# Kernel tuning notes

Measured on AMD Instinct MI355X. Metric: run time of the kernel, lower is better.

The kernel has to match this reference:

```python
import jax, jax.numpy as jnp
import numpy as np

B, H, S, D = 4, 16, 2048, 64


def setup_inputs() -> dict:
    key = jax.random.key(0)
    kq, kk, kv = jax.random.split(key, 3)
    q = jax.random.normal(kq, (B, H, S, D), dtype=jnp.float32)
    k = jax.random.normal(kk, (B, H, S, D), dtype=jnp.float32)
    v = jax.random.normal(kv, (B, H, S, D), dtype=jnp.float32)
    return {"q": q, "k": k, "v": v, "num_k": 170}


def reference(q, k, v, num_k):
    d_tensor = k.shape[-1]
    # [B,H,S,S] score matrix
    score = jnp.einsum("bhqd,bhkd->bhqk", q, k) / jnp.sqrt(jnp.float32(d_tensor))
    nk = min(int(num_k), k.shape[2])
    if nk:
        # kth-largest value per query row acts as threshold
        top_vals = jax.lax.top_k(score, nk)[0]          # [B,H,S,nk]
        thresh = top_vals[..., -1:]                      # [B,H,S,1]
        score = jnp.where(score < thresh, jnp.float32(-1e18), score)
    attn = jax.nn.softmax(score, axis=-1)
    return jnp.einsum("bhqk,bhkd->bhqd", attn, v)
```

## Files before the change

### kernel.cpp

```cpp
#include <hip/hip_runtime.h>
#include <math.h>

#define S_LEN 2048
#define DHEAD 64
#define NBINS 512
#define BPL (NBINS / 64)
#define CANDMAX 48
#define NBH 64
#define NROWS (NBH * S_LEN)
#define VT_BYTES (64ull * DHEAD * S_LEN * 2)

typedef _Float16 f16x8 __attribute__((ext_vector_type(8)));
typedef _Float16 f16x4 __attribute__((ext_vector_type(4)));
typedef float    f32x4 __attribute__((ext_vector_type(4)));

__global__ __launch_bounds__(256)
void prep_vt(const float* __restrict__ V, _Float16* __restrict__ VT) {
  __shared__ _Float16 trans[64][72];
  const int bh  = (int)blockIdx.x >> 5;
  const int kt  = (int)blockIdx.x & 31;
  const int t   = (int)threadIdx.x;
  const int key0 = kt * 64;
  const float* Vb = V + ((size_t)bh * S_LEN + key0) * DHEAD;

  {
    const int key = t >> 2;
    const int dc  = t & 3;
    #pragma unroll
    for (int i = 0; i < 4; ++i) {
      int d = dc * 16 + i * 4;
      float4 v4 = *(const float4*)(Vb + (size_t)key * DHEAD + d);
      trans[d + 0][key] = (_Float16)v4.x;
      trans[d + 1][key] = (_Float16)v4.y;
      trans[d + 2][key] = (_Float16)v4.z;
      trans[d + 3][key] = (_Float16)v4.w;
    }
  }
  __syncthreads();

  {
    const int dim = t >> 2;
    const int kc  = t & 3;
    _Float16* dst = VT + ((size_t)bh * DHEAD + dim) * S_LEN + key0 + kc * 16;
    f16x8 a, b;
    #pragma unroll
    for (int j = 0; j < 8; ++j) { a[j] = trans[dim][kc * 16 + j];
                                  b[j] = trans[dim][kc * 16 + 8 + j]; }
    *(f16x8*)(dst)     = a;
    *(f16x8*)(dst + 8) = b;
  }
}

__global__ __launch_bounds__(256, 4)
void qk_kernel(const float* __restrict__ Q, const float* __restrict__ K,
               float* __restrict__ Sws, int row0) {
  __shared__ __align__(16) char kbuf[32768];
  f16x8* Khw = (f16x8*)kbuf;
  f16x8* Klw = (f16x8*)(kbuf + 16384);

  const int tid  = (int)threadIdx.x;
  const int lane = tid & 63;
  const int wid  = tid >> 6;
  const int nxl  = (int)gridDim.x >> 3;
  const int xcd  = (int)blockIdx.x & 7;
  const int lb   = (int)blockIdx.x >> 3;
  const int rb   = lb >> 3;
  const int kb   = lb & 7;
  const int rowl = xcd * (nxl * 8) + rb * 64 + wid * 16;
  const int rowg = row0 + rowl;
  const int bh   = rowg >> 11;
  const int key0 = kb * 256;

  const int g = lane >> 4;
  const int m = lane & 15;

  f16x8 a_hi0, a_lo0, a_hi1, a_lo1;
  {
    const float* Qrow = Q + (size_t)(rowg + m) * DHEAD;
    float4 qa = *(const float4*)(Qrow + g * 8);
    float4 qb = *(const float4*)(Qrow + g * 8 + 4);
    float4 qc = *(const float4*)(Qrow + 32 + g * 8);
    float4 qd = *(const float4*)(Qrow + 32 + g * 8 + 4);
    float x[16] = {qa.x,qa.y,qa.z,qa.w, qb.x,qb.y,qb.z,qb.w,
                   qc.x,qc.y,qc.z,qc.w, qd.x,qd.y,qd.z,qd.w};
    #pragma unroll
    for (int j = 0; j < 8; ++j) {
      _Float16 h0 = (_Float16)x[j];
      a_hi0[j] = h0;  a_lo0[j] = (_Float16)(x[j] - (float)h0);
      _Float16 h1 = (_Float16)x[8 + j];
      a_hi1[j] = h1;  a_lo1[j] = (_Float16)(x[8 + j] - (float)h1);
    }
  }

  const float* Kb = K + (size_t)bh * (S_LEN * DHEAD);
  float* Srow = Sws + (size_t)rowl * S_LEN;

  const int skey  = tid >> 1;
  const int shalf = tid & 1;
  const int ssw   = skey & 7;

  float4 pf[8];
  {
    const float4* kr = (const float4*)(Kb + (size_t)(key0 + skey) * DHEAD + shalf * 32);
    #pragma unroll
    for (int j = 0; j < 8; ++j) pf[j] = kr[j];
  }

  #pragma unroll
  for (int t = 0; t < 2; ++t) {
    #pragma unroll
    for (int jj = 0; jj < 4; ++jj) {
      float x[8] = {pf[2*jj].x, pf[2*jj].y, pf[2*jj].z, pf[2*jj].w,
                    pf[2*jj+1].x, pf[2*jj+1].y, pf[2*jj+1].z, pf[2*jj+1].w};
      f16x8 hi, lo;
      #pragma unroll
      for (int j = 0; j < 8; ++j) {
        _Float16 h = (_Float16)x[j];
        hi[j] = h;
        lo[j] = (_Float16)(x[j] - (float)h);
      }
      int c = shalf * 4 + jj;
      Khw[skey * 8 + (c ^ ssw)] = hi;
      Klw[skey * 8 + (c ^ ssw)] = lo;
    }
    if (t + 1 < 2) {
      const float4* kr = (const float4*)(Kb + (size_t)(key0 + 128 + skey) * DHEAD + shalf * 32);
      #pragma unroll
      for (int j = 0; j < 8; ++j) pf[j] = kr[j];
    }
    __syncthreads();

    const f16x8* Kh = (const f16x8*)kbuf;
    const f16x8* Kl = (const f16x8*)(kbuf + 16384);
    int slot0 = ( g      ^ (m & 7));
    int slot1 = ((4 + g) ^ (m & 7));
    #pragma unroll
    for (int p = 0; p < 8; ++p) {
      int keyr = p * 16 + m;
      f16x8 b_hi0 = Kh[keyr * 8 + slot0];
      f16x8 b_hi1 = Kh[keyr * 8 + slot1];
      f16x8 b_lo0 = Kl[keyr * 8 + slot0];
      f16x8 b_lo1 = Kl[keyr * 8 + slot1];
      f32x4 acc = {0.f, 0.f, 0.f, 0.f};
      acc = __builtin_amdgcn_mfma_f32_16x16x32_f16(a_hi0, b_hi0, acc, 0, 0, 0);
      acc = __builtin_amdgcn_mfma_f32_16x16x32_f16(a_hi1, b_hi1, acc, 0, 0, 0);
      acc = __builtin_amdgcn_mfma_f32_16x16x32_f16(a_hi0, b_lo0, acc, 0, 0, 0);
      acc = __builtin_amdgcn_mfma_f32_16x16x32_f16(a_hi1, b_lo1, acc, 0, 0, 0);
      acc = __builtin_amdgcn_mfma_f32_16x16x32_f16(a_lo0, b_hi0, acc, 0, 0, 0);
      acc = __builtin_amdgcn_mfma_f32_16x16x32_f16(a_lo1, b_hi1, acc, 0, 0, 0);
      acc = __builtin_amdgcn_mfma_f32_16x16x32_f16(a_lo0, b_lo0, acc, 0, 0, 0);
      acc = __builtin_amdgcn_mfma_f32_16x16x32_f16(a_lo1, b_lo1, acc, 0, 0, 0);
      int col = key0 + t * 128 + p * 16 + m;
      #pragma unroll
      for (int rg = 0; rg < 4; ++rg)
        __builtin_nontemporal_store(acc[rg] * 0.125f,
            &Srow[(size_t)(g * 4 + rg) * S_LEN + col]);
    }
    __syncthreads();
  }
}

__global__ __launch_bounds__(512, 4)
void selmm_kernel(const float* __restrict__ Sws, const _Float16* __restrict__ VT,
                  const int* __restrict__ nkp, float* __restrict__ Out, int row0) {
  __shared__ unsigned histS[8][NBINS];
  __shared__ float candS[8][CANDMAX];
  __shared__ unsigned candCnt[8];
  __shared__ float psumS[16];
  __shared__ __align__(16) char pbuf[8192];
  __shared__ __align__(16) float4 redS[4][64];

  const int tid  = (int)threadIdx.x;
  const int lane = tid & 63;
  const int wid  = tid >> 6;
  const int nxl  = (int)gridDim.x >> 3;
  const int xcd  = (int)blockIdx.x & 7;
  const int lbk  = (int)blockIdx.x >> 3;
  const int rowlb = xcd * (nxl * 16) + lbk * 16;
  const int rowgb = row0 + rowlb;
  const int bh    = rowgb >> 11;

  int nk = nkp[0];
  if (nk > S_LEN) nk = S_LEN;

  unsigned* hw = histS[wid];
  float sarr[2][32];
  float thr2[2], vmx2[2];

  #pragma unroll
  for (int rr = 0; rr < 2; ++rr) {
    const int rloc = wid * 2 + rr;
    {
      const f32x4* S4 = (const f32x4*)(Sws + (size_t)(rowlb + rloc) * S_LEN);
      #pragma unroll
      for (int j = 0; j < 8; ++j) {
        f32x4 v4 = __builtin_nontemporal_load(S4 + j * 64 + lane);
        sarr[rr][j*4+0] = v4[0]; sarr[rr][j*4+1] = v4[1];
        sarr[rr][j*4+2] = v4[2]; sarr[rr][j*4+3] = v4[3];
      }
    }

    float vmax = -INFINITY, vmin = INFINITY;
    #pragma unroll
    for (int q = 0; q < 32; ++q) {
      vmax = fmaxf(vmax, sarr[rr][q]); vmin = fminf(vmin, sarr[rr][q]);
    }
    #pragma unroll
    for (int off = 32; off >= 1; off >>= 1) {
      vmax = fmaxf(vmax, __shfl_xor(vmax, off));
      vmin = fminf(vmin, __shfl_xor(vmin, off));
    }

    float thresh = -INFINITY;
    if (nk > 0) {
      float range = vmax - vmin;
      float scale = (range > 0.f) ? ((float)NBINS / range) : 0.f;
      float boff  = vmin * scale;

      #pragma unroll
      for (int i2 = 0; i2 < BPL; ++i2) hw[(i2 << 6) | lane] = 0u;
      #pragma unroll
      for (int q = 0; q < 32; ++q) {
        int bb = (int)fmaf(sarr[rr][q], scale, -boff);
        bb = bb < 0 ? 0 : (bb > NBINS - 1 ? NBINS - 1 : bb);
        atomicAdd(&hw[((bb & 7) << 6) | (bb >> 3)], 1u);
      }

      unsigned A = 0;
      #pragma unroll
      for (int i2 = 0; i2 < BPL; ++i2) A += hw[(i2 << 6) | lane];
      unsigned ssum = A;
      #pragma unroll
      for (int off = 1; off <= 32; off <<= 1) {
        unsigned u = (unsigned)__shfl_down((int)ssum, off);
        if (lane + off < 64) ssum += u;
      }
      unsigned cum = ssum - A;
      int bsel = -1; int mloc = 0; int nbloc = 0;
      #pragma unroll
      for (int i2 = BPL - 1; i2 >= 0; --i2) {
        unsigned c0 = cum; cum += hw[(i2 << 6) | lane];
        if (bsel < 0 && c0 < (unsigned)nk && cum >= (unsigned)nk) {
          bsel = (lane << 3) | i2; mloc = nk - (int)c0; nbloc = (int)(cum - c0);
        }
      }
      unsigned long long fm = __ballot(bsel >= 0);
      int srcl = __ffsll(fm) - 1;
      bsel = __shfl(bsel, srcl);
      int mth  = __shfl(mloc, srcl);
      int nbin = __shfl(nbloc, srcl);

      if (nbin <= CANDMAX) {
        if (lane == 0) candCnt[wid] = 0u;
        __builtin_amdgcn_wave_barrier();
        #pragma unroll
        for (int q = 0; q < 32; ++q) {
          int bb = (int)fmaf(sarr[rr][q], scale, -boff);
          bb = bb < 0 ? 0 : (bb > NBINS - 1 ? NBINS - 1 : bb);
          if (bb == bsel) {
            unsigned ix = atomicAdd(&candCnt[wid], 1u);
            if (ix < CANDMAX) candS[wid][ix] = sarr[rr][q];
          }
        }
        __builtin_amdgcn_wave_barrier();
        float prev = INFINITY, kth = -INFINITY;
        int got = 0, guard = 0;
        while (got < mth && guard++ <= CANDMAX) {
          float best = -INFINITY;
          for (int i = 0; i < nbin; ++i) {
            float v = candS[wid][i];
            if (v < prev && v > best) best = v;
          }
          int ce = 0;
          for (int i = 0; i < nbin; ++i) if (candS[wid][i] == best) ce++;
          got += ce; prev = best; kth = best;
        }
        thresh = kth;
      } else {
        unsigned inbin = 0;
        #pragma unroll
        for (int q = 0; q < 32; ++q) {
          int bb = (int)fmaf(sarr[rr][q], scale, -boff);
          bb = bb < 0 ? 0 : (bb > NBINS - 1 ? NBINS - 1 : bb);
          if (bb == bsel) inbin |= (1u << q);
        }
        while (true) {
          float cmax = -INFINITY;
          #pragma unroll
          for (int q = 0; q < 32; ++q) if (inbin & (1u << q)) cmax = fmaxf(cmax, sarr[rr][q]);
          #pragma unroll
          for (int off = 32; off >= 1; off >>= 1) cmax = fmaxf(cmax, __shfl_xor(cmax, off));
          int cnt = 0;
          #pragma unroll
          for (int q = 0; q < 32; ++q) if ((inbin & (1u << q)) && sarr[rr][q] == cmax) cnt++;
          #pragma unroll
          for (int off = 32; off >= 1; off >>= 1) cnt += __shfl_xor(cnt, off);
          if (mth <= cnt) { thresh = cmax; break; }
          mth -= cnt;
          #pragma unroll
          for (int q = 0; q < 32; ++q) if ((inbin & (1u << q)) && sarr[rr][q] == cmax) inbin &= ~(1u << q);
        }
      }
    }
    thr2[rr] = thresh; vmx2[rr] = vmax;

    float psum = 0.f;
    #pragma unroll
    for (int q = 0; q < 32; ++q) {
      float s = sarr[rr][q];
      psum += (s >= thresh) ? __expf(s - vmax) : 0.f;
    }
    #pragma unroll
    for (int off = 32; off >= 1; off >>= 1) psum += __shfl_xor(psum, off);
    if (lane == 0) psumS[rloc] = psum;
  }
  __syncthreads();

  const int g   = lane >> 4;
  const int n16 = lane & 15;
  const int dg  = wid & 3;
  const int kh  = wid >> 2;
  const _Float16* VTb = VT + (size_t)bh * (DHEAD * S_LEN);
  f32x4 acc = {0.f, 0.f, 0.f, 0.f};

  #pragma unroll
  for (int kt = 0; kt < 8; ++kt) {
    #pragma unroll
    for (int rr = 0; rr < 2; ++rr) {
      const int row = wid * 2 + rr;
      f16x4 pv;
      #pragma unroll
      for (int c = 0; c < 4; ++c) {
        float s = sarr[rr][kt * 4 + c];
        float p = (s >= thr2[rr]) ? __expf(s - vmx2[rr]) : 0.f;
        pv[c] = (_Float16)p;
      }
      *(f16x4*)(pbuf + ((row * 512 + lane * 8) ^ ((row & 7) << 4))) = pv;
    }
    __syncthreads();
    #pragma unroll
    for (int s = 0; s < 4; ++s) {
      f16x8 af = *(const f16x8*)(pbuf +
          ((n16 * 512 + kh * 256 + s * 64 + g * 16) ^ ((n16 & 7) << 4)));
      f16x8 bf = *(const f16x8*)(VTb + (size_t)(dg * 16 + n16) * S_LEN +
                                 kt * 256 + kh * 128 + s * 32 + g * 8);
      acc = __builtin_amdgcn_mfma_f32_16x16x32_f16(af, bf, acc, 0, 0, 0);
    }
    __syncthreads();
  }

  if (kh == 1) {
    redS[dg][lane] = make_float4(acc[0], acc[1], acc[2], acc[3]);
  }
  __syncthreads();
  if (kh == 0) {
    float4 o = redS[dg][lane];
    float ov[4] = {o.x, o.y, o.z, o.w};
    #pragma unroll
    for (int rg = 0; rg < 4; ++rg) {
      int row = g * 4 + rg;
      float val = (acc[rg] + ov[rg]) / psumS[row];
      Out[(size_t)(rowgb + row) * DHEAD + dg * 16 + n16] = val;
    }
  }
}

#define TQ 16
#define KT 128
#define NTILES (S_LEN / KT)
#define THREADS 512
#define LCAP 256
#define SOFF   0
#define KHI    131072
#define KLO    147456
#define HOFF   131072
#define KLOFF  147456
#define PLOFF  155648

__global__ __launch_bounds__(THREADS, 2)
void dpsa_kernel(const float* __restrict__ Q, const float* __restrict__ K,
                 const float* __restrict__ V, const int* __restrict__ nkp,
                 float* __restrict__ Out) {
  __shared__ __align__(16) char smem[163840];
  float* Sf = (float*)(smem + SOFF);

  const int tid  = (int)threadIdx.x;
  const int lane = tid & 63;
  const int wid  = tid >> 6;
  const int bid  = (int)blockIdx.x;
  const int bh   = bid >> 7;
  const int qblk = bid & 127;
  const size_t base = (size_t)bh * (size_t)(S_LEN * DHEAD);
  const float* Kbh = K + base;
  const float* Vbh = V + base;

  int nk = nkp[0];
  if (nk > S_LEN) nk = S_LEN;

  const int g = lane >> 4;
  const int m = lane & 15;

  f16x8 a_hi0, a_lo0, a_hi1, a_lo1;
  {
    const float* Qrow = Q + base + (size_t)(qblk * TQ + m) * DHEAD;
    float4 qa = *(const float4*)(Qrow + g * 8);
    float4 qb = *(const float4*)(Qrow + g * 8 + 4);
    float4 qc = *(const float4*)(Qrow + 32 + g * 8);
    float4 qd = *(const float4*)(Qrow + 32 + g * 8 + 4);
    float x[16] = {qa.x,qa.y,qa.z,qa.w, qb.x,qb.y,qb.z,qb.w,
                   qc.x,qc.y,qc.z,qc.w, qd.x,qd.y,qd.z,qd.w};
    #pragma unroll
    for (int j = 0; j < 8; ++j) {
      _Float16 h0 = (_Float16)x[j];
      a_hi0[j] = h0;  a_lo0[j] = (_Float16)(x[j] - (float)h0);
      _Float16 h1 = (_Float16)x[8 + j];
      a_hi1[j] = h1;  a_lo1[j] = (_Float16)(x[8 + j] - (float)h1);
    }
  }

  const f16x8* Kh = (const f16x8*)(smem + KHI);
  const f16x8* Kl = (const f16x8*)(smem + KLO);
  const int keyl = tid >> 2;
  const int q4i  = tid & 3;
  const int sw   = keyl & 7;

  float4 pf0, pf1, pf2, pf3;
  {
    const float4* Kg4 = (const float4*)Kbh;
    int idx = keyl * 16 + q4i * 4;
    pf0 = Kg4[idx]; pf1 = Kg4[idx + 1]; pf2 = Kg4[idx + 2]; pf3 = Kg4[idx + 3];
  }

  for (int t = 0; t < NTILES; ++t) {
    {
      float x[16] = {pf0.x,pf0.y,pf0.z,pf0.w, pf1.x,pf1.y,pf1.z,pf1.w,
                     pf2.x,pf2.y,pf2.z,pf2.w, pf3.x,pf3.y,pf3.z,pf3.w};
      f16x8 hi0, hi1, lo0, lo1;
      #pragma unroll
      for (int j = 0; j < 8; ++j) {
        _Float16 h0 = (_Float16)x[j];
        hi0[j] = h0;  lo0[j] = (_Float16)(x[j] - (float)h0);
        _Float16 h1 = (_Float16)x[8 + j];
        hi1[j] = h1;  lo1[j] = (_Float16)(x[8 + j] - (float)h1);
      }
      f16x8* KhwF = (f16x8*)(smem + KHI);
      f16x8* KlwF = (f16x8*)(smem + KLO);
      KhwF[keyl * 8 + ((q4i * 2)     ^ sw)] = hi0;
      KhwF[keyl * 8 + ((q4i * 2 + 1) ^ sw)] = hi1;
      KlwF[keyl * 8 + ((q4i * 2)     ^ sw)] = lo0;
      KlwF[keyl * 8 + ((q4i * 2 + 1) ^ sw)] = lo1;
    }
    if (t + 1 < NTILES) {
      const float4* Kg4 = (const float4*)(Kbh + (size_t)(t + 1) * (KT * DHEAD));
      int idx = keyl * 16 + q4i * 4;
      pf0 = Kg4[idx]; pf1 = Kg4[idx + 1]; pf2 = Kg4[idx + 2]; pf3 = Kg4[idx + 3];
    }
    __syncthreads();
    {
      int keyr = wid * 16 + m;
      int s0 = ( g      ^ (m & 7));
      int s1 = ((4 + g) ^ (m & 7));
      f16x8 b_hi0 = Kh[keyr * 8 + s0];
      f16x8 b_hi1 = Kh[keyr * 8 + s1];
      f16x8 b_lo0 = Kl[keyr * 8 + s0];
      f16x8 b_lo1 = Kl[keyr * 8 + s1];
      f32x4 acc = {0.f, 0.f, 0.f, 0.f};
      acc = __builtin_amdgcn_mfma_f32_16x16x32_f16(a_hi0, b_hi0, acc, 0, 0, 0);
      acc = __builtin_amdgcn_mfma_f32_16x16x32_f16(a_hi1, b_hi1, acc, 0, 0, 0);
      acc = __builtin_amdgcn_mfma_f32_16x16x32_f16(a_hi0, b_lo0, acc, 0, 0, 0);
      acc = __builtin_amdgcn_mfma_f32_16x16x32_f16(a_hi1, b_lo1, acc, 0, 0, 0);
      acc = __builtin_amdgcn_mfma_f32_16x16x32_f16(a_lo0, b_hi0, acc, 0, 0, 0);
      acc = __builtin_amdgcn_mfma_f32_16x16x32_f16(a_lo1, b_hi1, acc, 0, 0, 0);
      int keyabs = t * KT + wid * 16 + m;
      #pragma unroll
      for (int rg = 0; rg < 4; ++rg)
        Sf[(size_t)(g * 4 + rg) * S_LEN + keyabs] = acc[rg] * 0.125f;
    }
    __syncthreads();
  }

  unsigned* hw = (unsigned*)(smem + HOFF)  + wid * NBINS;
  unsigned* kl = (unsigned*)(smem + KLOFF) + wid * LCAP;
  float*    pl = (float*)(smem + PLOFF)    + wid * LCAP;
  const float4* S4 = (const float4*)(smem + SOFF);

  for (int rr = 0; rr < 2; ++rr) {
    const int row = wid * 2 + rr;
    float sarr[32];
    #pragma unroll
    for (int j = 0; j < 8; ++j) {
      float4 v4 = S4[row * (S_LEN / 4) + j * 64 + lane];
      sarr[j*4+0] = v4.x; sarr[j*4+1] = v4.y;
      sarr[j*4+2] = v4.z; sarr[j*4+3] = v4.w;
    }

    float vmax = -INFINITY, vmin = INFINITY;
    #pragma unroll
    for (int q = 0; q < 32; ++q) {
      vmax = fmaxf(vmax, sarr[q]); vmin = fminf(vmin, sarr[q]);
    }
    #pragma unroll
    for (int off = 32; off >= 1; off >>= 1) {
      vmax = fmaxf(vmax, __shfl_xor(vmax, off));
      vmin = fminf(vmin, __shfl_xor(vmin, off));
    }

    float thresh = -INFINITY;
    if (nk > 0) {
      float range = vmax - vmin;
      float scale = (range > 0.f) ? ((float)NBINS / range) : 0.f;
      #pragma unroll
      for (int i2 = 0; i2 < BPL; ++i2) hw[(i2 << 6) | lane] = 0u;
      #pragma unroll
      for (int q = 0; q < 32; ++q) {
        int bb = (int)((sarr[q] - vmin) * scale);
        bb = bb < 0 ? 0 : (bb > NBINS - 1 ? NBINS - 1 : bb);
        atomicAdd(&hw[((bb & 7) << 6) | (bb >> 3)], 1u);
      }
      unsigned A = 0; unsigned hv[BPL];
      #pragma unroll
      for (int i2 = 0; i2 < BPL; ++i2) { hv[i2] = hw[(i2 << 6) | lane]; A += hv[i2]; }
      unsigned ssum = A;
      #pragma unroll
      for (int off = 1; off <= 32; off <<= 1) {
        unsigned u = (unsigned)__shfl_down((int)ssum, off);
        if (lane + off < 64) ssum += u;
      }
      unsigned cum = ssum - A;
      int bsel = -1; int mloc = 0;
      #pragma unroll
      for (int i2 = BPL - 1; i2 >= 0; --i2) {
        unsigned c0 = cum; cum += hv[i2];
        if (bsel < 0 && c0 < (unsigned)nk && cum >= (unsigned)nk) {
          bsel = (lane << 3) | i2; mloc = nk - (int)c0;
        }
      }
      unsigned long long fmk = __ballot(bsel >= 0);
      int srcl = __ffsll(fmk) - 1;
      bsel = __shfl(bsel, srcl);
      int mth = __shfl(mloc, srcl);

      unsigned inbin = 0;
      #pragma unroll
      for (int q = 0; q < 32; ++q) {
        int bb = (int)((sarr[q] - vmin) * scale);
        bb = bb < 0 ? 0 : (bb > NBINS - 1 ? NBINS - 1 : bb);
        if (bb == bsel) inbin |= (1u << q);
      }
      while (true) {
        float cmax = -INFINITY;
        #pragma unroll
        for (int q = 0; q < 32; ++q) if (inbin & (1u << q)) cmax = fmaxf(cmax, sarr[q]);
        #pragma unroll
        for (int off = 32; off >= 1; off >>= 1) cmax = fmaxf(cmax, __shfl_xor(cmax, off));
        int cnt = 0;
        #pragma unroll
        for (int q = 0; q < 32; ++q) if ((inbin & (1u << q)) && sarr[q] == cmax) cnt++;
        #pragma unroll
        for (int off = 32; off >= 1; off >>= 1) cnt += __shfl_xor(cnt, off);
        if (mth <= cnt) { thresh = cmax; break; }
        mth -= cnt;
        #pragma unroll
        for (int q = 0; q < 32; ++q) if ((inbin & (1u << q)) && sarr[q] == cmax) inbin &= ~(1u << q);
      }
    }

    float psum = 0.f;
    #pragma unroll
    for (int q = 0; q < 32; ++q) {
      float p = (sarr[q] >= thresh) ? expf(sarr[q] - vmax) : 0.f;
      sarr[q] = p; psum += p;
    }
    #pragma unroll
    for (int off = 32; off >= 1; off >>= 1) psum += __shfl_xor(psum, off);

    unsigned nkept = 0;
    #pragma unroll
    for (int q = 0; q < 32; ++q) {
      bool keep = sarr[q] > 0.f;
      unsigned long long mk = __ballot(keep);
      if (keep) {
        unsigned idx = nkept + (unsigned)__popcll(mk & ((1ull << lane) - 1ull));
        if (idx < LCAP) {
          kl[idx] = (unsigned)((q >> 2) * 256 + lane * 4 + (q & 3));
          pl[idx] = sarr[q];
        }
      }
      nkept += (unsigned)__popcll(mk);
    }

    float acc0 = 0.f, acc1 = 0.f, acc2 = 0.f, acc3 = 0.f;
    if (nkept <= LCAP) {
      unsigned i = 0;
      for (; i + 4 <= nkept; i += 4) {
        acc0 = fmaf(pl[i+0], Vbh[(size_t)kl[i+0] * DHEAD + lane], acc0);
        acc1 = fmaf(pl[i+1], Vbh[(size_t)kl[i+1] * DHEAD + lane], acc1);
        acc2 = fmaf(pl[i+2], Vbh[(size_t)kl[i+2] * DHEAD + lane], acc2);
        acc3 = fmaf(pl[i+3], Vbh[(size_t)kl[i+3] * DHEAD + lane], acc3);
      }
      for (; i < nkept; ++i)
        acc0 = fmaf(pl[i], Vbh[(size_t)kl[i] * DHEAD + lane], acc0);
    } else {
      #pragma unroll
      for (int q = 0; q < 32; ++q) {
        for (int sl = 0; sl < 64; ++sl) {
          float pp = __shfl(sarr[q], sl);
          if (pp > 0.f)
            acc0 = fmaf(pp, Vbh[(size_t)((q >> 2) * 256 + sl * 4 + (q & 3)) * DHEAD + lane], acc0);
        }
      }
    }
    float accv = (acc0 + acc1) + (acc2 + acc3);
    Out[base + (size_t)(qblk * TQ + row) * DHEAD + lane] = accv / psum;
  }
}

extern "C" void kernel_launch(void* const* d_in, const int* in_sizes, int n_in,
                              void* d_out, int out_size, void* d_ws, size_t ws_size,
                              hipStream_t stream) {
  const float* q  = (const float*)d_in[0];
  const float* k  = (const float*)d_in[1];
  const float* v  = (const float*)d_in[2];
  const int*   nk = (const int*)d_in[3];
  float* out = (float*)d_out;

  size_t srem = (ws_size > VT_BYTES) ? (ws_size - VT_BYTES) : 0;
  size_t maxrows = srem / ((size_t)S_LEN * sizeof(float));
  long long chunk = (long long)(maxrows / 512) * 512;
  if (chunk > NROWS) chunk = NROWS;

  if (chunk >= 512) {
    _Float16* vt = (_Float16*)d_ws;
    float* sws = (float*)((char*)d_ws + VT_BYTES);
    prep_vt<<<dim3(2048), dim3(256), 0, stream>>>(v, vt);
    for (int row0 = 0; row0 < NROWS; row0 += (int)chunk) {
      int rows = (NROWS - row0 < (int)chunk) ? (NROWS - row0) : (int)chunk;
      qk_kernel<<<dim3(rows / 8), dim3(256), 0, stream>>>(q, k, sws, row0);
      selmm_kernel<<<dim3(rows / 16), dim3(512), 0, stream>>>(sws, vt, nk, out, row0);
    }
  } else {
    dpsa_kernel<<<dim3(8192), dim3(THREADS), 0, stream>>>(q, k, v, nk, out);
  }
}
```

Baseline: 874.2 us.

## Use one wave per row in selmm with 1024-thread blocks and 4-way K split

The selection and PV kernel now runs 16 waves per block, one score row per wave, where before 8 waves each handled two rows serially. The PV matmul is split four ways over the key dimension and the partial sums are reduced through shared memory. Shared buffers are aliased into one union to fit 16 per-wave histograms. This roughly halves the per-wave register array and serial threshold work, trading it for more threads per block, a lower blocks-per-CU bound, and a larger cross-wave reduction.

After: 1.044 ms. 19.4% more time.

```diff
diff --git a/kernel.cpp b/kernel.cpp
--- a/kernel.cpp
+++ b/kernel.cpp
@@ -37,7 +37,6 @@
     }
   }
   __syncthreads();
-
   {
     const int dim = t >> 2;
     const int kc  = t & 3;
@@ -160,15 +159,16 @@
   }
 }
 
-__global__ __launch_bounds__(512, 4)
+__global__ __launch_bounds__(1024, 2)
 void selmm_kernel(const float* __restrict__ Sws, const _Float16* __restrict__ VT,
                   const int* __restrict__ nkp, float* __restrict__ Out, int row0) {
-  __shared__ unsigned histS[8][NBINS];
-  __shared__ float candS[8][CANDMAX];
-  __shared__ unsigned candCnt[8];
-  __shared__ float psumS[16];
-  __shared__ __align__(16) char pbuf[8192];
-  __shared__ __align__(16) float4 redS[4][64];
+  __shared__ __align__(16) char smem[35968];
+  unsigned* histS  = (unsigned*)smem;
+  char*     pbuf   = smem;
+  float4*   redS   = (float4*)(smem + 8192);
+  float*    candS  = (float*)(smem + 32768);
+  unsigned* candCnt= (unsigned*)(smem + 35840);
+  float*    psumS  = (float*)(smem + 35904);
 
   const int tid  = (int)threadIdx.x;
   const int lane = tid & 63;
@@ -183,183 +183,185 @@
   int nk = nkp[0];
   if (nk > S_LEN) nk = S_LEN;
 
-  unsigned* hw = histS[wid];
-  float sarr[2][32];
-  float thr2[2], vmx2[2];
-
+  unsigned* hw = histS + wid * NBINS;
+  float*    cw = candS + wid * CANDMAX;
+  float sarr[32];
+  float thr, vmx;
+
+  {
+    const f32x4* S4 = (const f32x4*)(Sws + (size_t)(rowlb + wid) * S_LEN);
+    #pragma unroll
+    for (int j = 0; j < 8; ++j) {
+      f32x4 v4 = __builtin_nontemporal_load(S4 + j * 64 + lane);
+      sarr[j*4+0] = v4[0]; sarr[j*4+1] = v4[1];
+      sarr[j*4+2] = v4[2]; sarr[j*4+3] = v4[3];
+    }
+  }
+
+  float vmax = -INFINITY, vmin = INFINITY;
   #pragma unroll
-  for (int rr = 0; rr < 2; ++rr) {
-    const int rloc = wid * 2 + rr;
-    {
-      const f32x4* S4 = (const f32x4*)(Sws + (size_t)(rowlb + rloc) * S_LEN);
-      #pragma unroll
-      for (int j = 0; j < 8; ++j) {
-        f32x4 v4 = __builtin_nontemporal_load(S4 + j * 64 + lane);
-        sarr[rr][j*4+0] = v4[0]; sarr[rr][j*4+1] = v4[1];
-        sarr[rr][j*4+2] = v4[2]; sarr[rr][j*4+3] = v4[3];
-      }
-    }
-
-    float vmax = -INFINITY, vmin = INFINITY;
+  for (int q = 0; q < 32; ++q) {
+    vmax = fmaxf(vmax, sarr[q]); vmin = fminf(vmin, sarr[q]);
+  }
+  #pragma unroll
+  for (int off = 32; off >= 1; off >>= 1) {
+    vmax = fmaxf(vmax, __shfl_xor(vmax, off));
+    vmin = fminf(vmin, __shfl_xor(vmin, off));
+  }
+
+  float thresh = -INFINITY;
+  if (nk > 0) {
+    float range = vmax - vmin;
+    float scale = (range > 0.f) ? ((float)NBINS / range) : 0.f;
+    float boff  = vmin * scale;
+
+    #pragma unroll
+    for (int i2 = 0; i2 < BPL; ++i2) hw[(i2 << 6) | lane] = 0u;
     #pragma unroll
     for (int q = 0; q < 32; ++q) {
-      vmax = fmaxf(vmax, sarr[rr][q]); vmin = fminf(vmin, sarr[rr][q]);
-    }
-    #pragma unroll
-    for (int off = 32; off >= 1; off >>= 1) {
-      vmax = fmaxf(vmax, __shfl_xor(vmax, off));
-      vmin = fminf(vmin, __shfl_xor(vmin, off));
-    }
-
-    float thresh = -INFINITY;
-    if (nk > 0) {
-      float range = vmax - vmin;
-      float scale = (range > 0.f) ? ((float)NBINS / range) : 0.f;
-      float boff  = vmin * scale;
-
-      #pragma unroll
-      for (int i2 = 0; i2 < BPL; ++i2) hw[(i2 << 6) | lane] = 0u;
+      int bb = (int)fmaf(sarr[q], scale, -boff);
+      bb = bb < 0 ? 0 : (bb > NBINS - 1 ? NBINS - 1 : bb);
+      atomicAdd(&hw[((bb & 7) << 6) | (bb >> 3)], 1u);
+    }
+
+    unsigned A = 0;
+    #pragma unroll
+    for (int i2 = 0; i2 < BPL; ++i2) A += hw[(i2 << 6) | lane];
+    unsigned ssum = A;
+    #pragma unroll
+    for (int off = 1; off <= 32; off <<= 1) {
+      unsigned u = (unsigned)__shfl_down((int)ssum, off);
+      if (lane + off < 64) ssum += u;
+    }
+    unsigned cum = ssum - A;
+    int bsel = -1; int mloc = 0; int nbloc = 0;
+    #pragma unroll
+    for (int i2 = BPL - 1; i2 >= 0; --i2) {
+      unsigned c0 = cum; cum += hw[(i2 << 6) | lane];
+      if (bsel < 0 && c0 < (unsigned)nk && cum >= (unsigned)nk) {
+        bsel = (lane << 3) | i2; mloc = nk - (int)c0; nbloc = (int)(cum - c0);
+      }
+    }
+    unsigned long long fm = __ballot(bsel >= 0);
+    int srcl = __ffsll(fm) - 1;
+    bsel = __shfl(bsel, srcl);
+    int mth  = __shfl(mloc, srcl);
+    int nbin = __shfl(nbloc, srcl);
+
+    if (nbin <= CANDMAX) {
+      if (lane == 0) candCnt[wid] = 0u;
+      __builtin_amdgcn_wave_barrier();
       #pragma unroll
       for (int q = 0; q < 32; ++q) {
-        int bb = (int)fmaf(sarr[rr][q], scale, -boff);
+        int bb = (int)fmaf(sarr[q], scale, -boff);
         bb = bb < 0 ? 0 : (bb > NBINS - 1 ? NBINS - 1 : bb);
-        atomicAdd(&hw[((bb & 7) << 6) | (bb >> 3)], 1u);
-      }
-
-      unsigned A = 0;
-      #pragma unroll
-      for (int i2 = 0; i2 < BPL; ++i2) A += hw[(i2 << 6) | lane];
-      unsigned ssum = A;
-      #pragma unroll
-      for (int off = 1; off <= 32; off <<= 1) {
-        unsigned u = (unsigned)__shfl_down((int)ssum, off);
-        if (lane + off < 64) ssum += u;
-      }
-      unsigned cum = ssum - A;
-      int bsel = -1; int mloc = 0; int nbloc = 0;
-      #pragma unroll
-      for (int i2 = BPL - 1; i2 >= 0; --i2) {
-        unsigned c0 = cum; cum += hw[(i2 << 6) | lane];
-        if (bsel < 0 && c0 < (unsigned)nk && cum >= (unsigned)nk) {
-          bsel = (lane << 3) | i2; mloc = nk - (int)c0; nbloc = (int)(cum - c0);
+        if (bb == bsel) {
+          unsigned ix = atomicAdd(&candCnt[wid], 1u);
+          if (ix < CANDMAX) cw[ix] = sarr[q];
         }
       }
-      unsigned long long fm = __ballot(bsel >= 0);
-      int srcl = __ffsll(fm) - 1;
-      bsel = __shfl(bsel, srcl);
-      int mth  = __shfl(mloc, srcl);
-      int nbin = __shfl(nbloc, srcl);
-
-      if (nbin <= CANDMAX) {
-        if (lane == 0) candCnt[wid] = 0u;
-        __builtin_amdgcn_wave_barrier();
-        #pragma unroll
-        for (int q = 0; q < 32; ++q) {
-          int bb = (int)fmaf(sarr[rr][q], scale, -boff);
-          bb = bb < 0 ? 0 : (bb > NBINS - 1 ? NBINS - 1 : bb);
-          if (bb == bsel) {
-            unsigned ix = atomicAdd(&candCnt[wid], 1u);
-            if (ix < CANDMAX) candS[wid][ix] = sarr[rr][q];
-          }
+      __builtin_amdgcn_wave_barrier();
+      float prev = INFINITY, kth = -INFINITY;
+      int got = 0, guard = 0;
+      while (got < mth && guard++ <= CANDMAX) {
+        float best = -INFINITY;
+        for (int i = 0; i < nbin; ++i) {
+          float v = cw[i];
+          if (v < prev && v > best) best = v;
         }
-        __builtin_amdgcn_wave_barrier();
-        float prev = INFINITY, kth = -INFINITY;
-        int got = 0, guard = 0;
-        while (got < mth && guard++ <= CANDMAX) {
-          float best = -INFINITY;
-          for (int i = 0; i < nbin; ++i) {
-            float v = candS[wid][i];
-            if (v < prev && v > best) best = v;
-          }
-          int ce = 0;
-          for (int i = 0; i < nbin; ++i) if (candS[wid][i] == best) ce++;
-          got += ce; prev = best; kth = best;
-        }
-        thresh = kth;
-      } else {
-        unsigned inbin = 0;
-        #pragma unroll
-        for (int q = 0; q < 32; ++q) {
-          int bb = (int)fmaf(sarr[rr][q], scale, -boff);
-          bb = bb < 0 ? 0 : (bb > NBINS - 1 ? NBINS - 1 : bb);
-          if (bb == bsel) inbin |= (1u << q);
-        }
-        while (true) {
-          float cmax = -INFINITY;
-          #pragma unroll
-          for (int q = 0; q < 32; ++q) if (inbin & (1u << q)) cmax = fmaxf(cmax, sarr[rr][q]);
-          #pragma unroll
-          for (int off = 32; off >= 1; off >>= 1) cmax = fmaxf(cmax, __shfl_xor(cmax, off));
-          int cnt = 0;
-          #pragma unroll
-          for (int q = 0; q < 32; ++q) if ((inbin & (1u << q)) && sarr[rr][q] == cmax) cnt++;
-          #pragma unroll
-          for (int off = 32; off >= 1; off >>= 1) cnt += __shfl_xor(cnt, off);
-          if (mth <= cnt) { thresh = cmax; break; }
-          mth -= cnt;
-          #pragma unroll
-          for (int q = 0; q < 32; ++q) if ((inbin & (1u << q)) && sarr[rr][q] == cmax) inbin &= ~(1u << q);
-        }
-      }
-    }
-    thr2[rr] = thresh; vmx2[rr] = vmax;
-
+        int ce = 0;
+        for (int i = 0; i < nbin; ++i) if (cw[i] == best) ce++;
+        got += ce; prev = best; kth = best;
+      }
+      thresh = kth;
+    } else {
+      unsigned inbin = 0;
+      #pragma unroll
+      for (int q = 0; q < 32; ++q) {
+        int bb = (int)fmaf(sarr[q], scale, -boff);
+        bb = bb < 0 ? 0 : (bb > NBINS - 1 ? NBINS - 1 : bb);
+        if (bb == bsel) inbin |= (1u << q);
+      }
+      while (true) {
+        float cmax = -INFINITY;
+        #pragma unroll
+        for (int q = 0; q < 32; ++q) if (inbin & (1u << q)) cmax = fmaxf(cmax, sarr[q]);
+        #pragma unroll
+        for (int off = 32; off >= 1; off >>= 1) cmax = fmaxf(cmax, __shfl_xor(cmax, off));
+        int cnt = 0;
+        #pragma unroll
+        for (int q = 0; q < 32; ++q) if ((inbin & (1u << q)) && sarr[q] == cmax) cnt++;
+        #pragma unroll
+        for (int off = 32; off >= 1; off >>= 1) cnt += __shfl_xor(cnt, off);
+        if (mth <= cnt) { thresh = cmax; break; }
+        mth -= cnt;
+        #pragma unroll
+        for (int q = 0; q < 32; ++q) if ((inbin & (1u << q)) && sarr[q] == cmax) inbin &= ~(1u << q);
+      }
+    }
+  }
+  thr = thresh; vmx = vmax;
+
+  {
     float psum = 0.f;
     #pragma unroll
     for (int q = 0; q < 32; ++q) {
-      float s = sarr[rr][q];
-      psum += (s >= thresh) ? __expf(s - vmax) : 0.f;
+      float s = sarr[q];
+      psum += (s >= thr) ? __expf(s - vmx) : 0.f;
     }
     #pragma unroll
     for (int off = 32; off >= 1; off >>= 1) psum += __shfl_xor(psum, off);
-    if (lane == 0) psumS[rloc] = psum;
+    if (lane == 0) psumS[wid] = psum;
   }
   __syncthreads();
 
   const int g   = lane >> 4;
   const int n16 = lane & 15;
+  const int kq  = wid >> 2;
   const int dg  = wid & 3;
-  const int kh  = wid >> 2;
   const _Float16* VTb = VT + (size_t)bh * (DHEAD * S_LEN);
   f32x4 acc = {0.f, 0.f, 0.f, 0.f};
 
   #pragma unroll
   for (int kt = 0; kt < 8; ++kt) {
-    #pragma unroll
-    for (int rr = 0; rr < 2; ++rr) {
-      const int row = wid * 2 + rr;
+    {
       f16x4 pv;
       #pragma unroll
       for (int c = 0; c < 4; ++c) {
-        float s = sarr[rr][kt * 4 + c];
-        float p = (s >= thr2[rr]) ? __expf(s - vmx2[rr]) : 0.f;
+        float s = sarr[kt * 4 + c];
+        float p = (s >= thr) ? __expf(s - vmx) : 0.f;
         pv[c] = (_Float16)p;
       }
-      *(f16x4*)(pbuf + ((row * 512 + lane * 8) ^ ((row & 7) << 4))) = pv;
+      *(f16x4*)(pbuf + ((wid * 512 + lane * 8) ^ ((wid & 7) << 4))) = pv;
     }
     __syncthreads();
     #pragma unroll
-    for (int s = 0; s < 4; ++s) {
+    for (int s2 = 0; s2 < 2; ++s2) {
+      int slice = kq * 2 + s2;
       f16x8 af = *(const f16x8*)(pbuf +
-          ((n16 * 512 + kh * 256 + s * 64 + g * 16) ^ ((n16 & 7) << 4)));
+          ((n16 * 512 + slice * 64 + g * 16) ^ ((n16 & 7) << 4)));
       f16x8 bf = *(const f16x8*)(VTb + (size_t)(dg * 16 + n16) * S_LEN +
-                                 kt * 256 + kh * 128 + s * 32 + g * 8);
+                                 kt * 256 + kq * 64 + s2 * 32 + g * 8);
       acc = __builtin_amdgcn_mfma_f32_16x16x32_f16(af, bf, acc, 0, 0, 0);
     }
     __syncthreads();
   }
 
-  if (kh == 1) {
-    redS[dg][lane] = make_float4(acc[0], acc[1], acc[2], acc[3]);
+  if (kq > 0) {
+    redS[((kq - 1) * 4 + dg) * 64 + lane] = make_float4(acc[0], acc[1], acc[2], acc[3]);
   }
   __syncthreads();
-  if (kh == 0) {
-    float4 o = redS[dg][lane];
-    float ov[4] = {o.x, o.y, o.z, o.w};
+  if (kq == 0) {
+    float tot[4] = {acc[0], acc[1], acc[2], acc[3]};
+    #pragma unroll
+    for (int p = 0; p < 3; ++p) {
+      float4 o = redS[(p * 4 + dg) * 64 + lane];
+      tot[0] += o.x; tot[1] += o.y; tot[2] += o.z; tot[3] += o.w;
+    }
     #pragma unroll
     for (int rg = 0; rg < 4; ++rg) {
       int row = g * 4 + rg;
-      float val = (acc[rg] + ov[rg]) / psumS[row];
+      float val = tot[rg] / psumS[row];
       Out[(size_t)(rowgb + row) * DHEAD + dg * 16 + n16] = val;
     }
   }
@@ -636,7 +638,7 @@
     for (int row0 = 0; row0 < NROWS; row0 += (int)chunk) {
       int rows = (NROWS - row0 < (int)chunk) ? (NROWS - row0) : (int)chunk;
       qk_kernel<<<dim3(rows / 8), dim3(256), 0, stream>>>(q, k, sws, row0);
-      selmm_kernel<<<dim3(rows / 16), dim3(512), 0, stream>>>(sws, vt, nk, out, row0);
+      selmm_kernel<<<dim3(rows / 16), dim3(1024), 0, stream>>>(sws, vt, nk, out, row0);
     }
   } else {
     dpsa_kernel<<<dim3(8192), dim3(THREADS), 0, stream>>>(q, k, v, nk, out);
```
